# Kernel optimization log

Measured on AMD Instinct MI355X. Metric: run time of the kernel, lower is better.

## Reference

```python
import jax, jax.numpy as jnp
import numpy as np

NUM_HEADS = 12
LN_EPS = 1e-5


def _layernorm(x, w, b):
    m = jnp.mean(x, axis=-1, keepdims=True)
    v = jnp.mean(jnp.square(x - m), axis=-1, keepdims=True)
    return (x - m) * jax.lax.rsqrt(v + LN_EPS) * w + b


def setup_inputs() -> dict:
    key = jax.random.key(0)
    ks = jax.random.split(key, 6)
    B, N, C, H = 8, 1024, 768, 3072
    s = 0.02
    return {
        "x": jax.random.normal(ks[0], (B, N, C), jnp.float32),
        "ln1_w": jnp.ones((C,), jnp.float32),
        "ln1_b": jnp.zeros((C,), jnp.float32),
        "qkv_w": jax.random.normal(ks[1], (3 * C, C), jnp.float32) * s,
        "qkv_b": jnp.zeros((3 * C,), jnp.float32),
        "proj_w": jax.random.normal(ks[2], (C, C), jnp.float32) * s,
        "proj_b": jnp.zeros((C,), jnp.float32),
        "ln2_w": jnp.ones((C,), jnp.float32),
        "ln2_b": jnp.zeros((C,), jnp.float32),
        "fc1_w": jax.random.normal(ks[3], (H, C), jnp.float32) * s,
        "fc1_b": jnp.zeros((H,), jnp.float32),
        "fc2_w": jax.random.normal(ks[4], (C, H), jnp.float32) * s,
        "fc2_b": jnp.zeros((C,), jnp.float32),
    }


def reference(x, ln1_w, ln1_b, qkv_w, qkv_b, proj_w, proj_b,
              ln2_w, ln2_b, fc1_w, fc1_b, fc2_w, fc2_b):
    B, N, C = x.shape
    H = NUM_HEADS
    d = C // H
    scale = d ** (-0.5)

    # --- attention on norm1(x) (size=None path, dropout rates are 0) ---
    h = _layernorm(x, ln1_w, ln1_b)
    qkv = h @ qkv_w.T + qkv_b                      # [B,N,3C]
    qkv = qkv.reshape(B, N, 3, H, d).transpose(2, 0, 3, 1, 4)  # [3,B,H,N,d]
    q, k, v = qkv[0], qkv[1], qkv[2]
    attn = jnp.einsum('bhqd,bhkd->bhqk', q, k) * scale
    attn = jax.nn.softmax(attn, axis=-1)
    o = jnp.einsum('bhqk,bhkd->bhqd', attn, v)     # [B,H,N,d]
    o = o.transpose(0, 2, 1, 3).reshape(B, N, C)
    x_attn = o @ proj_w.T + proj_b

    # --- residual + MLP ---
    x = x + x_attn
    h2 = _layernorm(x, ln2_w, ln2_b)
    h2 = jax.nn.gelu(h2 @ fc1_w.T + fc1_b, approximate=False)
    x = x + (h2 @ fc2_w.T + fc2_b)
    return x
```

## Files before the change

### kernel.cpp

```cpp
#include <hip/hip_runtime.h>
#include <cmath>

typedef __bf16 bf16;
typedef __bf16 bf16x8 __attribute__((ext_vector_type(8)));
typedef __bf16 bf16x4 __attribute__((ext_vector_type(4)));
typedef float floatx4 __attribute__((ext_vector_type(4)));

#define MFMA16(A, B, C) __builtin_amdgcn_mfma_f32_16x16x32_bf16((A), (B), (C), 0, 0, 0)

#define GLDS16(g, l)                                                   \
  __builtin_amdgcn_global_load_lds(                                    \
      (const __attribute__((address_space(1))) void*)(g),              \
      (__attribute__((address_space(3))) void*)(l), 16, 0, 0)

__global__ __launch_bounds__(256) void pre_kernel(
    const float* __restrict__ x, const float* __restrict__ g,
    const float* __restrict__ be, bf16* __restrict__ h1,
    const float* __restrict__ s0, bf16* __restrict__ d0, int n0,
    const float* __restrict__ s1, bf16* __restrict__ d1, int n1,
    const float* __restrict__ s2, bf16* __restrict__ d2, int n2,
    const float* __restrict__ s3, bf16* __restrict__ d3, int n3) {
  int bid = blockIdx.x;
  int t = threadIdx.x;
  if (bid < 8192) {
    const float* xr = x + (size_t)bid * 768;
    float v0 = xr[t], v1 = xr[t + 256], v2 = xr[t + 512];
    float s = v0 + v1 + v2;
    float s2 = v0 * v0 + v1 * v1 + v2 * v2;
#pragma unroll
    for (int o = 1; o < 64; o <<= 1) {
      s += __shfl_xor(s, o, 64);
      s2 += __shfl_xor(s2, o, 64);
    }
    __shared__ float red[8];
    int w = t >> 6, lane = t & 63;
    if (lane == 0) { red[w] = s; red[4 + w] = s2; }
    __syncthreads();
    float ts = red[0] + red[1] + red[2] + red[3];
    float ts2 = red[4] + red[5] + red[6] + red[7];
    float mean = ts * (1.0f / 768.0f);
    float var = ts2 * (1.0f / 768.0f) - mean * mean;
    float rstd = rsqrtf(var + 1e-5f);
    bf16* orow = h1 + (size_t)bid * 768;
    orow[t]       = (bf16)((v0 - mean) * rstd * g[t]       + be[t]);
    orow[t + 256] = (bf16)((v1 - mean) * rstd * g[t + 256] + be[t + 256]);
    orow[t + 512] = (bf16)((v2 - mean) * rstd * g[t + 512] + be[t + 512]);
    return;
  }
  int i = (bid - 8192) * 256 + t;
  const float* s;
  bf16* d;
  if (i < n0) { s = s0 + (size_t)i * 4; d = d0 + (size_t)i * 4; }
  else if ((i -= n0) < n1) { s = s1 + (size_t)i * 4; d = d1 + (size_t)i * 4; }
  else if ((i -= n1) < n2) { s = s2 + (size_t)i * 4; d = d2 + (size_t)i * 4; }
  else if ((i -= n2) < n3) { s = s3 + (size_t)i * 4; d = d3 + (size_t)i * 4; }
  else return;
  bf16x4 v;
  v[0] = (bf16)s[0]; v[1] = (bf16)s[1]; v[2] = (bf16)s[2]; v[3] = (bf16)s[3];
  *(bf16x4*)d = v;
}

__global__ __launch_bounds__(256) void reduce_ln_kernel(
    const bf16* __restrict__ pp, const float* __restrict__ bias,
    const float* __restrict__ x, const float* __restrict__ g,
    const float* __restrict__ be, float* __restrict__ x1,
    bf16* __restrict__ h2) {
  int row = blockIdx.x;
  int t = threadIdx.x;
  const bf16* p0 = pp + (size_t)row * 768;
  const bf16* p1 = pp + (size_t)(8192 + row) * 768;
  const float* xr = x + (size_t)row * 768;
  float v0 = (float)p0[t]       + (float)p1[t]       + bias[t]       + xr[t];
  float v1 = (float)p0[t + 256] + (float)p1[t + 256] + bias[t + 256] + xr[t + 256];
  float v2 = (float)p0[t + 512] + (float)p1[t + 512] + bias[t + 512] + xr[t + 512];
  float* x1r = x1 + (size_t)row * 768;
  x1r[t] = v0; x1r[t + 256] = v1; x1r[t + 512] = v2;
  float s = v0 + v1 + v2;
  float s2 = v0 * v0 + v1 * v1 + v2 * v2;
#pragma unroll
  for (int o = 1; o < 64; o <<= 1) {
    s += __shfl_xor(s, o, 64);
    s2 += __shfl_xor(s2, o, 64);
  }
  __shared__ float red[8];
  int w = t >> 6, lane = t & 63;
  if (lane == 0) { red[w] = s; red[4 + w] = s2; }
  __syncthreads();
  float ts = red[0] + red[1] + red[2] + red[3];
  float ts2 = red[4] + red[5] + red[6] + red[7];
  float mean = ts * (1.0f / 768.0f);
  float var = ts2 * (1.0f / 768.0f) - mean * mean;
  float rstd = rsqrtf(var + 1e-5f);
  bf16* orow = h2 + (size_t)row * 768;
  orow[t]       = (bf16)((v0 - mean) * rstd * g[t]       + be[t]);
  orow[t + 256] = (bf16)((v1 - mean) * rstd * g[t + 256] + be[t + 256]);
  orow[t + 512] = (bf16)((v2 - mean) * rstd * g[t + 512] + be[t + 512]);
}

__global__ __launch_bounds__(256) void reduce_out_kernel(
    const bf16* __restrict__ pp, const float* __restrict__ bias,
    const float* __restrict__ x1, float* __restrict__ out) {
  int i = blockIdx.x * 256 + threadIdx.x;
  size_t base = (size_t)i * 4;
  int col = (int)(base % 768);
  bf16x4 a = *(const bf16x4*)(pp + base);
  bf16x4 b = *(const bf16x4*)(pp + (size_t)8192 * 768 + base);
  float4 xr = *(const float4*)(x1 + base);
  float4 r;
  r.x = (float)a[0] + (float)b[0] + bias[col]     + xr.x;
  r.y = (float)a[1] + (float)b[1] + bias[col + 1] + xr.y;
  r.z = (float)a[2] + (float)b[2] + bias[col + 2] + xr.z;
  r.w = (float)a[3] + (float)b[3] + bias[col + 3] + xr.w;
  *(float4*)(out + base) = r;
}

constexpr int EP_BF16 = 0;
constexpr int EP_PART = 1;
constexpr int EP_GELU_BF16 = 2;

template <int EP>
__global__ __launch_bounds__(256, 3) void gemm_bt(
    const bf16* __restrict__ A, const bf16* __restrict__ Bw,
    const float* __restrict__ bias,
    void* __restrict__ outp, int M, int N, int K) {
  __shared__ alignas(16) bf16 Asl[128 * 64];
  __shared__ alignas(16) bf16 Bsl[128 * 64];
  int tid = threadIdx.x;
  int lane = tid & 63, w = tid >> 6;
  int wm = w >> 1, wn = w & 1;
  int q16 = lane & 15, quad = lane >> 4;
  int fid = blockIdx.x + gridDim.x * blockIdx.y;
  int nb = gridDim.x;
  int s = fid >> 3;
  int m0 = ((fid & 7) * (gridDim.y >> 3) + s / nb) * 128;
  int n0 = (s % nb) * 128;
  int kz = blockIdx.z;
  int Ksub = K / gridDim.z;
  int kbeg = kz * Ksub;

  floatx4 acc[4][4];
#pragma unroll
  for (int i = 0; i < 4; i++)
#pragma unroll
    for (int j = 0; j < 4; j++) acc[i][j] = (floatx4){0.f, 0.f, 0.f, 0.f};

  int rIn = lane >> 3;
  int cg = (lane & 7) ^ rIn;
  const bf16* ag[4];
  const bf16* bg[4];
#pragma unroll
  for (int q = 0; q < 4; q++) {
    int ca = w * 4 + q;
    ag[q] = A + (size_t)(m0 + ca * 8 + rIn) * K + kbeg + cg * 8;
    bg[q] = Bw + (size_t)(n0 + ca * 8 + rIn) * K + kbeg + cg * 8;
  }
  bf16* la = &Asl[w * 2048];
  bf16* lb = &Bsl[w * 2048];

  int msel = q16 & 7;
  int offA[2][4], offB[2][4];
#pragma unroll
  for (int ks = 0; ks < 2; ks++) {
#pragma unroll
    for (int i = 0; i < 4; i++) {
      offA[ks][i] = (wm * 64 + i * 16 + q16) * 64 + (((ks * 4 + quad) ^ msel)) * 8;
      offB[ks][i] = (wn * 64 + i * 16 + q16) * 64 + (((ks * 4 + quad) ^ msel)) * 8;
    }
  }

  for (int k0 = 0; k0 < Ksub; k0 += 64) {
    __syncthreads();
#pragma unroll
    for (int q = 0; q < 4; q++) {
      GLDS16(ag[q], la + q * 512);
      GLDS16(bg[q], lb + q * 512);
      ag[q] += 64;
      bg[q] += 64;
    }
    __syncthreads();
#pragma unroll
    for (int ks = 0; ks < 2; ks++) {
      bf16x8 af[4], bfr[4];
#pragma unroll
      for (int i = 0; i < 4; i++) af[i] = *(const bf16x8*)&Asl[offA[ks][i]];
#pragma unroll
      for (int j = 0; j < 4; j++) bfr[j] = *(const bf16x8*)&Bsl[offB[ks][j]];
#pragma unroll
      for (int i = 0; i < 4; i++)
#pragma unroll
        for (int j = 0; j < 4; j++) acc[i][j] = MFMA16(af[i], bfr[j], acc[i][j]);
    }
  }

  bf16* opart = (bf16*)outp + (size_t)kz * M * N;
#pragma unroll
  for (int i = 0; i < 4; i++) {
#pragma unroll
    for (int j = 0; j < 4; j++) {
#pragma unroll
      for (int r = 0; r < 4; r++) {
        int m = m0 + wm * 64 + i * 16 + quad * 4 + r;
        int n = n0 + wn * 64 + j * 16 + q16;
        size_t idx = (size_t)m * N + n;
        if constexpr (EP == EP_PART) {
          opart[idx] = (bf16)acc[i][j][r];
        } else {
          float v = acc[i][j][r] + bias[n];
          if constexpr (EP == EP_BF16) {
            ((bf16*)outp)[idx] = (bf16)v;
          } else {
            float u = v * (2.3022083f + 0.1029443f * v * v);
            float e = __builtin_amdgcn_exp2f(-u);
            float gv = v * __builtin_amdgcn_rcpf(1.0f + e);
            ((bf16*)outp)[idx] = (bf16)gv;
          }
        }
      }
    }
  }
}

__global__ __launch_bounds__(256, 3) void attn_kernel(const bf16* __restrict__ qkv,
                                                      bf16* __restrict__ o) {
  __shared__ alignas(16) bf16 Kl[32 * 64];
  __shared__ alignas(16) bf16 Vt[64 * 5 * 8];
  __shared__ alignas(16) bf16 Pl[4][2][16 * 40];
  int tid = threadIdx.x;
  int lane = tid & 63, w = tid >> 6;
  int q16 = lane & 15, quad = lane >> 4;
  int b = blockIdx.y / 12, h = blockIdx.y % 12;
  int qbase = blockIdx.x * 128 + w * 32;

  bf16x8 qf[2][2];
#pragma unroll
  for (int qt = 0; qt < 2; qt++)
#pragma unroll
    for (int c = 0; c < 2; c++)
      qf[qt][c] = *(const bf16x8*)(qkv +
          (size_t)(b * 1024 + qbase + qt * 16 + q16) * 2304 + h * 64 +
          c * 32 + quad * 8);

  int kkey = w * 8 + (lane >> 3);
  int kchunk = (lane & 7) ^ (lane >> 3);
  const bf16* kg = qkv + (size_t)(b * 1024 + kkey) * 2304 + 768 + h * 64 +
                   (kchunk & 7) * 8;
  bf16* kl_dst = &Kl[w * 512];

  int kr = tid >> 3;
  int kcb = (tid & 7) * 8;
  const bf16* vg = qkv + (size_t)(b * 1024 + kr) * 2304 + 1536 + h * 64 + kcb;
  int vt_idx[8];
#pragma unroll
  for (int e = 0; e < 8; e++)
    vt_idx[e] = ((((kcb + e) * 5) + w) ^ (tid & 7)) * 8 + (kr & 7);

  int koff[2][2];
#pragma unroll
  for (int nc = 0; nc < 2; nc++)
#pragma unroll
    for (int ck = 0; ck < 2; ck++) {
      int key = nc * 16 + q16;
      koff[nc][ck] = (key * 8 + ((ck * 4 + quad) ^ (key & 7))) * 8;
    }
  int voff[4];
#pragma unroll
  for (int dc = 0; dc < 4; dc++) {
    int d = dc * 16 + q16;
    voff[dc] = ((d * 5 + quad) ^ ((d >> 3) & 7)) * 8;
  }
  const bf16* pread = &Pl[w][0][q16 * 40 + quad * 8];
  int pw_base = (quad * 4) * 40 + q16;

  float l_[2][4];
  floatx4 oacc[2][4];
#pragma unroll
  for (int qt = 0; qt < 2; qt++)
#pragma unroll
    for (int r = 0; r < 4; r++) l_[qt][r] = 0.f;
#pragma unroll
  for (int qt = 0; qt < 2; qt++)
#pragma unroll
    for (int dc = 0; dc < 4; dc++) oacc[qt][dc] = (floatx4){0.f, 0.f, 0.f, 0.f};

  for (int kt = 0; kt < 32; kt++) {
    __syncthreads();
    GLDS16(kg, kl_dst);
    bf16x8 vv = *(const bf16x8*)vg;
    kg += 32 * 2304;
    vg += 32 * 2304;
#pragma unroll
    for (int e = 0; e < 8; e++) Vt[vt_idx[e]] = vv[e];
    __syncthreads();

    bf16x8 kf[2][2];
#pragma unroll
    for (int nc = 0; nc < 2; nc++)
#pragma unroll
      for (int ck = 0; ck < 2; ck++)
        kf[nc][ck] = *(const bf16x8*)&Kl[koff[nc][ck]];

#pragma unroll
    for (int qt = 0; qt < 2; qt++) {
#pragma unroll
      for (int nc = 0; nc < 2; nc++) {
        floatx4 z = (floatx4){0.f, 0.f, 0.f, 0.f};
        z = MFMA16(qf[qt][0], kf[nc][0], z);
        z = MFMA16(qf[qt][1], kf[nc][1], z);
#pragma unroll
        for (int r = 0; r < 4; r++) {
          float p = __builtin_amdgcn_exp2f(z[r] * 0.18033688011f);
          l_[qt][r] += p;
          Pl[w][qt][pw_base + r * 40 + nc * 16] = (bf16)p;
        }
      }
    }
    __syncthreads();

    bf16x8 vf[4];
#pragma unroll
    for (int dc = 0; dc < 4; dc++) vf[dc] = *(const bf16x8*)&Vt[voff[dc]];
#pragma unroll
    for (int qt = 0; qt < 2; qt++) {
      bf16x8 pf = *(const bf16x8*)(pread + qt * 640);
#pragma unroll
      for (int dc = 0; dc < 4; dc++)
        oacc[qt][dc] = MFMA16(pf, vf[dc], oacc[qt][dc]);
    }
  }

#pragma unroll
  for (int qt = 0; qt < 2; qt++) {
    bf16* op = o + (size_t)(b * 1024 + qbase + qt * 16) * 768 + h * 64;
#pragma unroll
    for (int r = 0; r < 4; r++) {
      float s = l_[qt][r];
#pragma unroll
      for (int off = 1; off < 16; off <<= 1) s += __shfl_xor(s, off, 16);
      float inv = 1.0f / s;
#pragma unroll
      for (int dc = 0; dc < 4; dc++)
        op[(size_t)(quad * 4 + r) * 768 + dc * 16 + q16] =
            (bf16)(oacc[qt][dc][r] * inv);
    }
  }
}

extern "C" void kernel_launch(void* const* d_in, const int* in_sizes, int n_in,
                              void* d_out, int out_size, void* d_ws, size_t ws_size,
                              hipStream_t stream) {
  (void)in_sizes; (void)n_in; (void)out_size; (void)ws_size;
  const float* x      = (const float*)d_in[0];
  const float* ln1_w  = (const float*)d_in[1];
  const float* ln1_b  = (const float*)d_in[2];
  const float* qkv_w  = (const float*)d_in[3];
  const float* qkv_b  = (const float*)d_in[4];
  const float* proj_w = (const float*)d_in[5];
  const float* proj_b = (const float*)d_in[6];
  const float* ln2_w  = (const float*)d_in[7];
  const float* ln2_b  = (const float*)d_in[8];
  const float* fc1_w  = (const float*)d_in[9];
  const float* fc1_b  = (const float*)d_in[10];
  const float* fc2_w  = (const float*)d_in[11];
  const float* fc2_b  = (const float*)d_in[12];

  char* ws = (char*)d_ws;
  size_t off = 0;
  auto alloc = [&](size_t bytes) {
    void* p = ws + off;
    off += (bytes + 255) & ~(size_t)255;
    return p;
  };
  bf16* wq  = (bf16*)alloc((size_t)2304 * 768 * 2);
  bf16* wp  = (bf16*)alloc((size_t)768 * 768 * 2);
  bf16* wf1 = (bf16*)alloc((size_t)3072 * 768 * 2);
  bf16* wf2 = (bf16*)alloc((size_t)768 * 3072 * 2);
  bf16* slotA = (bf16*)alloc((size_t)8192 * 768 * 2);
  bf16* slotB = (bf16*)alloc((size_t)8192 * 3072 * 2);
  float* x1 = (float*)alloc((size_t)8192 * 768 * 4);
  bf16* part = (bf16*)alloc((size_t)2 * 8192 * 768 * 2);

  bf16* h1 = slotA;
  bf16* qkvb = slotB;
  bf16* ob = slotA;
  bf16* h2 = slotA;
  bf16* hm = slotB;

  pre_kernel<<<8192 + 6912, 256, 0, stream>>>(
      x, ln1_w, ln1_b, h1,
      qkv_w, wq, 2304 * 768 / 4, proj_w, wp, 768 * 768 / 4,
      fc1_w, wf1, 3072 * 768 / 4, fc2_w, wf2, 768 * 3072 / 4);

  gemm_bt<EP_BF16><<<dim3(18, 64, 1), 256, 0, stream>>>(h1, wq, qkv_b, qkvb,
                                                        8192, 2304, 768);
  attn_kernel<<<dim3(8, 96), 256, 0, stream>>>(qkvb, ob);
  gemm_bt<EP_PART><<<dim3(6, 64, 2), 256, 0, stream>>>(ob, wp, nullptr, part,
                                                       8192, 768, 768);
  reduce_ln_kernel<<<8192, 256, 0, stream>>>(part, proj_b, x, ln2_w, ln2_b,
                                             x1, h2);
  gemm_bt<EP_GELU_BF16><<<dim3(24, 64, 1), 256, 0, stream>>>(h2, wf1, fc1_b, hm,
                                                             8192, 3072, 768);
  gemm_bt<EP_PART><<<dim3(6, 64, 2), 256, 0, stream>>>(hm, wf2, nullptr, part,
                                                       8192, 768, 3072);
  reduce_out_kernel<<<6144, 256, 0, stream>>>(part, fc2_b, x1, (float*)d_out);
}
```

Baseline: 334.2 us.

## Replace split-K partials with 128x64 tiles, fuse residual epilogue, widen attention KV tile

The proj and fc2 GEMMs drop split-K, which wrote bf16 partials that a separate reduce kernel then summed. They now use 128x64 output tiles, templated via NJ, so the grid stays large, and add bias plus residual in the epilogue, writing fp32 directly. The reduce kernels are removed, leaving a plain LayerNorm kernel on x1. Attention now processes 64 keys per iteration with double K/V buffers, removes one barrier per step, and remaps blocks so each batch sits on one XCD. Risks are lower arithmetic intensity from the narrower tiles, and possible races on the P buffer now that the barrier between P write and read is gone, though each warp reads only its own region.

Measured after the change: 332.2 us. About the same (-0.6%).

```diff
diff --git a/kernel.cpp b/kernel.cpp
--- a/kernel.cpp
+++ b/kernel.cpp
@@ -60,21 +60,14 @@
   *(bf16x4*)d = v;
 }
 
-__global__ __launch_bounds__(256) void reduce_ln_kernel(
-    const bf16* __restrict__ pp, const float* __restrict__ bias,
-    const float* __restrict__ x, const float* __restrict__ g,
-    const float* __restrict__ be, float* __restrict__ x1,
-    bf16* __restrict__ h2) {
+__global__ __launch_bounds__(256) void ln_kernel(const float* __restrict__ x,
+                                                 const float* __restrict__ g,
+                                                 const float* __restrict__ be,
+                                                 bf16* __restrict__ out) {
   int row = blockIdx.x;
   int t = threadIdx.x;
-  const bf16* p0 = pp + (size_t)row * 768;
-  const bf16* p1 = pp + (size_t)(8192 + row) * 768;
   const float* xr = x + (size_t)row * 768;
-  float v0 = (float)p0[t]       + (float)p1[t]       + bias[t]       + xr[t];
-  float v1 = (float)p0[t + 256] + (float)p1[t + 256] + bias[t + 256] + xr[t + 256];
-  float v2 = (float)p0[t + 512] + (float)p1[t + 512] + bias[t + 512] + xr[t + 512];
-  float* x1r = x1 + (size_t)row * 768;
-  x1r[t] = v0; x1r[t + 256] = v1; x1r[t + 512] = v2;
+  float v0 = xr[t], v1 = xr[t + 256], v2 = xr[t + 512];
   float s = v0 + v1 + v2;
   float s2 = v0 * v0 + v1 * v1 + v2 * v2;
 #pragma unroll
@@ -91,40 +84,23 @@
   float mean = ts * (1.0f / 768.0f);
   float var = ts2 * (1.0f / 768.0f) - mean * mean;
   float rstd = rsqrtf(var + 1e-5f);
-  bf16* orow = h2 + (size_t)row * 768;
+  bf16* orow = out + (size_t)row * 768;
   orow[t]       = (bf16)((v0 - mean) * rstd * g[t]       + be[t]);
   orow[t + 256] = (bf16)((v1 - mean) * rstd * g[t + 256] + be[t + 256]);
   orow[t + 512] = (bf16)((v2 - mean) * rstd * g[t + 512] + be[t + 512]);
 }
 
-__global__ __launch_bounds__(256) void reduce_out_kernel(
-    const bf16* __restrict__ pp, const float* __restrict__ bias,
-    const float* __restrict__ x1, float* __restrict__ out) {
-  int i = blockIdx.x * 256 + threadIdx.x;
-  size_t base = (size_t)i * 4;
-  int col = (int)(base % 768);
-  bf16x4 a = *(const bf16x4*)(pp + base);
-  bf16x4 b = *(const bf16x4*)(pp + (size_t)8192 * 768 + base);
-  float4 xr = *(const float4*)(x1 + base);
-  float4 r;
-  r.x = (float)a[0] + (float)b[0] + bias[col]     + xr.x;
-  r.y = (float)a[1] + (float)b[1] + bias[col + 1] + xr.y;
-  r.z = (float)a[2] + (float)b[2] + bias[col + 2] + xr.z;
-  r.w = (float)a[3] + (float)b[3] + bias[col + 3] + xr.w;
-  *(float4*)(out + base) = r;
-}
-
 constexpr int EP_BF16 = 0;
-constexpr int EP_PART = 1;
+constexpr int EP_RES_F32 = 1;
 constexpr int EP_GELU_BF16 = 2;
 
-template <int EP>
+template <int EP, int NJ>
 __global__ __launch_bounds__(256, 3) void gemm_bt(
     const bf16* __restrict__ A, const bf16* __restrict__ Bw,
-    const float* __restrict__ bias,
+    const float* __restrict__ bias, const float* __restrict__ resid,
     void* __restrict__ outp, int M, int N, int K) {
   __shared__ alignas(16) bf16 Asl[128 * 64];
-  __shared__ alignas(16) bf16 Bsl[128 * 64];
+  __shared__ alignas(16) bf16 Bsl[NJ * 32 * 64];
   int tid = threadIdx.x;
   int lane = tid & 63, w = tid >> 6;
   int wm = w >> 1, wn = w & 1;
@@ -133,87 +109,85 @@
   int nb = gridDim.x;
   int s = fid >> 3;
   int m0 = ((fid & 7) * (gridDim.y >> 3) + s / nb) * 128;
-  int n0 = (s % nb) * 128;
-  int kz = blockIdx.z;
-  int Ksub = K / gridDim.z;
-  int kbeg = kz * Ksub;
-
-  floatx4 acc[4][4];
+  int n0 = (s % nb) * (NJ * 32);
+
+  floatx4 acc[4][NJ];
 #pragma unroll
   for (int i = 0; i < 4; i++)
 #pragma unroll
-    for (int j = 0; j < 4; j++) acc[i][j] = (floatx4){0.f, 0.f, 0.f, 0.f};
+    for (int j = 0; j < NJ; j++) acc[i][j] = (floatx4){0.f, 0.f, 0.f, 0.f};
 
   int rIn = lane >> 3;
   int cg = (lane & 7) ^ rIn;
   const bf16* ag[4];
-  const bf16* bg[4];
-#pragma unroll
-  for (int q = 0; q < 4; q++) {
-    int ca = w * 4 + q;
-    ag[q] = A + (size_t)(m0 + ca * 8 + rIn) * K + kbeg + cg * 8;
-    bg[q] = Bw + (size_t)(n0 + ca * 8 + rIn) * K + kbeg + cg * 8;
-  }
+  const bf16* bg[NJ];
+#pragma unroll
+  for (int q = 0; q < 4; q++)
+    ag[q] = A + (size_t)(m0 + (w * 4 + q) * 8 + rIn) * K + cg * 8;
+#pragma unroll
+  for (int q = 0; q < NJ; q++)
+    bg[q] = Bw + (size_t)(n0 + (w * NJ + q) * 8 + rIn) * K + cg * 8;
   bf16* la = &Asl[w * 2048];
-  bf16* lb = &Bsl[w * 2048];
+  bf16* lb = &Bsl[w * NJ * 512];
 
   int msel = q16 & 7;
-  int offA[2][4], offB[2][4];
+  int offA[2][4], offB[2][NJ];
 #pragma unroll
   for (int ks = 0; ks < 2; ks++) {
 #pragma unroll
-    for (int i = 0; i < 4; i++) {
+    for (int i = 0; i < 4; i++)
       offA[ks][i] = (wm * 64 + i * 16 + q16) * 64 + (((ks * 4 + quad) ^ msel)) * 8;
-      offB[ks][i] = (wn * 64 + i * 16 + q16) * 64 + (((ks * 4 + quad) ^ msel)) * 8;
-    }
-  }
-
-  for (int k0 = 0; k0 < Ksub; k0 += 64) {
+#pragma unroll
+    for (int j = 0; j < NJ; j++)
+      offB[ks][j] = (wn * 16 * NJ + j * 16 + q16) * 64 + (((ks * 4 + quad) ^ msel)) * 8;
+  }
+
+  for (int k0 = 0; k0 < K; k0 += 64) {
     __syncthreads();
 #pragma unroll
     for (int q = 0; q < 4; q++) {
       GLDS16(ag[q], la + q * 512);
+      ag[q] += 64;
+    }
+#pragma unroll
+    for (int q = 0; q < NJ; q++) {
       GLDS16(bg[q], lb + q * 512);
-      ag[q] += 64;
       bg[q] += 64;
     }
     __syncthreads();
 #pragma unroll
     for (int ks = 0; ks < 2; ks++) {
-      bf16x8 af[4], bfr[4];
+      bf16x8 af[4], bfr[NJ];
 #pragma unroll
       for (int i = 0; i < 4; i++) af[i] = *(const bf16x8*)&Asl[offA[ks][i]];
 #pragma unroll
-      for (int j = 0; j < 4; j++) bfr[j] = *(const bf16x8*)&Bsl[offB[ks][j]];
+      for (int j = 0; j < NJ; j++) bfr[j] = *(const bf16x8*)&Bsl[offB[ks][j]];
 #pragma unroll
       for (int i = 0; i < 4; i++)
 #pragma unroll
-        for (int j = 0; j < 4; j++) acc[i][j] = MFMA16(af[i], bfr[j], acc[i][j]);
-    }
-  }
-
-  bf16* opart = (bf16*)outp + (size_t)kz * M * N;
+        for (int j = 0; j < NJ; j++) acc[i][j] = MFMA16(af[i], bfr[j], acc[i][j]);
+    }
+  }
+
 #pragma unroll
   for (int i = 0; i < 4; i++) {
 #pragma unroll
-    for (int j = 0; j < 4; j++) {
+    for (int j = 0; j < NJ; j++) {
 #pragma unroll
       for (int r = 0; r < 4; r++) {
         int m = m0 + wm * 64 + i * 16 + quad * 4 + r;
-        int n = n0 + wn * 64 + j * 16 + q16;
+        int n = n0 + wn * 16 * NJ + j * 16 + q16;
         size_t idx = (size_t)m * N + n;
-        if constexpr (EP == EP_PART) {
-          opart[idx] = (bf16)acc[i][j][r];
+        float v = acc[i][j][r] + bias[n];
+        if constexpr (EP == EP_BF16) {
+          ((bf16*)outp)[idx] = (bf16)v;
+        } else if constexpr (EP == EP_RES_F32) {
+          ((float*)outp)[idx] = v + resid[idx];
         } else {
-          float v = acc[i][j][r] + bias[n];
-          if constexpr (EP == EP_BF16) {
-            ((bf16*)outp)[idx] = (bf16)v;
-          } else {
-            float u = v * (2.3022083f + 0.1029443f * v * v);
-            float e = __builtin_amdgcn_exp2f(-u);
-            float gv = v * __builtin_amdgcn_rcpf(1.0f + e);
-            ((bf16*)outp)[idx] = (bf16)gv;
-          }
+          float u = v * (2.3022083f + 0.1029443f * v * v);
+          float e = __builtin_amdgcn_exp2f(-u);
+          float gv = v * __builtin_amdgcn_rcpf(1.0f + e);
+          ((bf16*)outp)[idx] = (bf16)gv;
         }
       }
     }
@@ -222,14 +196,16 @@
 
 __global__ __launch_bounds__(256, 3) void attn_kernel(const bf16* __restrict__ qkv,
                                                       bf16* __restrict__ o) {
-  __shared__ alignas(16) bf16 Kl[32 * 64];
-  __shared__ alignas(16) bf16 Vt[64 * 5 * 8];
-  __shared__ alignas(16) bf16 Pl[4][2][16 * 40];
+  __shared__ alignas(16) bf16 Kl[2][32 * 64];
+  __shared__ alignas(16) bf16 Vt[2][64 * 40];
+  __shared__ alignas(16) bf16 Pl[4][2][16 * 68];
   int tid = threadIdx.x;
   int lane = tid & 63, w = tid >> 6;
   int q16 = lane & 15, quad = lane >> 4;
-  int b = blockIdx.y / 12, h = blockIdx.y % 12;
-  int qbase = blockIdx.x * 128 + w * 32;
+  int f = blockIdx.x;
+  int xcd = f & 7, idx = f >> 3;
+  int b = xcd, h = idx % 12;
+  int qbase = (idx / 12) * 128 + w * 32;
 
   bf16x8 qf[2][2];
 #pragma unroll
@@ -242,17 +218,20 @@
 
   int kkey = w * 8 + (lane >> 3);
   int kchunk = (lane & 7) ^ (lane >> 3);
-  const bf16* kg = qkv + (size_t)(b * 1024 + kkey) * 2304 + 768 + h * 64 +
-                   (kchunk & 7) * 8;
-  bf16* kl_dst = &Kl[w * 512];
+  const bf16* kg0 = qkv + (size_t)(b * 1024 + kkey) * 2304 + 768 + h * 64 +
+                    kchunk * 8;
+  const bf16* kg1 = kg0 + 32 * 2304;
+  bf16* kd0 = &Kl[0][w * 512];
+  bf16* kd1 = &Kl[1][w * 512];
 
   int kr = tid >> 3;
   int kcb = (tid & 7) * 8;
-  const bf16* vg = qkv + (size_t)(b * 1024 + kr) * 2304 + 1536 + h * 64 + kcb;
+  const bf16* vg0 = qkv + (size_t)(b * 1024 + kr) * 2304 + 1536 + h * 64 + kcb;
+  const bf16* vg1 = vg0 + 32 * 2304;
   int vt_idx[8];
 #pragma unroll
   for (int e = 0; e < 8; e++)
-    vt_idx[e] = ((((kcb + e) * 5) + w) ^ (tid & 7)) * 8 + (kr & 7);
+    vt_idx[e] = ((((kcb + e) * 5) + (kr >> 3)) ^ (tid & 7)) * 8 + (kr & 7);
 
   int koff[2][2];
 #pragma unroll
@@ -268,8 +247,8 @@
     int d = dc * 16 + q16;
     voff[dc] = ((d * 5 + quad) ^ ((d >> 3) & 7)) * 8;
   }
-  const bf16* pread = &Pl[w][0][q16 * 40 + quad * 8];
-  int pw_base = (quad * 4) * 40 + q16;
+  const bf16* pread = &Pl[w][0][q16 * 68 + quad * 8];
+  int pw_base = (quad * 4) * 68 + q16;
 
   float l_[2][4];
   floatx4 oacc[2][4];
@@ -282,27 +261,31 @@
 #pragma unroll
     for (int dc = 0; dc < 4; dc++) oacc[qt][dc] = (floatx4){0.f, 0.f, 0.f, 0.f};
 
-  for (int kt = 0; kt < 32; kt++) {
-    __syncthreads();
-    GLDS16(kg, kl_dst);
-    bf16x8 vv = *(const bf16x8*)vg;
-    kg += 32 * 2304;
-    vg += 32 * 2304;
-#pragma unroll
-    for (int e = 0; e < 8; e++) Vt[vt_idx[e]] = vv[e];
-    __syncthreads();
-
-    bf16x8 kf[2][2];
-#pragma unroll
-    for (int nc = 0; nc < 2; nc++)
+  for (int kt = 0; kt < 16; kt++) {
+    __syncthreads();
+    GLDS16(kg0, kd0);
+    GLDS16(kg1, kd1);
+    bf16x8 vv0 = *(const bf16x8*)vg0;
+    bf16x8 vv1 = *(const bf16x8*)vg1;
+    kg0 += 64 * 2304; kg1 += 64 * 2304;
+    vg0 += 64 * 2304; vg1 += 64 * 2304;
+#pragma unroll
+    for (int e = 0; e < 8; e++) Vt[0][vt_idx[e]] = vv0[e];
+#pragma unroll
+    for (int e = 0; e < 8; e++) Vt[1][vt_idx[e]] = vv1[e];
+    __syncthreads();
+
+    bf16x8 kf[4][2];
+#pragma unroll
+    for (int nc = 0; nc < 4; nc++)
 #pragma unroll
       for (int ck = 0; ck < 2; ck++)
-        kf[nc][ck] = *(const bf16x8*)&Kl[koff[nc][ck]];
+        kf[nc][ck] = *(const bf16x8*)&Kl[nc >> 1][koff[nc & 1][ck]];
 
 #pragma unroll
     for (int qt = 0; qt < 2; qt++) {
 #pragma unroll
-      for (int nc = 0; nc < 2; nc++) {
+      for (int nc = 0; nc < 4; nc++) {
         floatx4 z = (floatx4){0.f, 0.f, 0.f, 0.f};
         z = MFMA16(qf[qt][0], kf[nc][0], z);
         z = MFMA16(qf[qt][1], kf[nc][1], z);
@@ -310,21 +293,26 @@
         for (int r = 0; r < 4; r++) {
           float p = __builtin_amdgcn_exp2f(z[r] * 0.18033688011f);
           l_[qt][r] += p;
-          Pl[w][qt][pw_base + r * 40 + nc * 16] = (bf16)p;
+          Pl[w][qt][pw_base + r * 68 + nc * 16] = (bf16)p;
         }
       }
     }
-    __syncthreads();
-
-    bf16x8 vf[4];
-#pragma unroll
-    for (int dc = 0; dc < 4; dc++) vf[dc] = *(const bf16x8*)&Vt[voff[dc]];
+
+    bf16x8 vf[2][4];
+#pragma unroll
+    for (int kh = 0; kh < 2; kh++)
+#pragma unroll
+      for (int dc = 0; dc < 4; dc++)
+        vf[kh][dc] = *(const bf16x8*)&Vt[kh][voff[dc]];
 #pragma unroll
     for (int qt = 0; qt < 2; qt++) {
-      bf16x8 pf = *(const bf16x8*)(pread + qt * 640);
-#pragma unroll
-      for (int dc = 0; dc < 4; dc++)
-        oacc[qt][dc] = MFMA16(pf, vf[dc], oacc[qt][dc]);
+#pragma unroll
+      for (int kh = 0; kh < 2; kh++) {
+        bf16x8 pf = *(const bf16x8*)(pread + qt * 1088 + kh * 32);
+#pragma unroll
+        for (int dc = 0; dc < 4; dc++)
+          oacc[qt][dc] = MFMA16(pf, vf[kh][dc], oacc[qt][dc]);
+      }
     }
   }
 
@@ -377,7 +365,6 @@
   bf16* slotA = (bf16*)alloc((size_t)8192 * 768 * 2);
   bf16* slotB = (bf16*)alloc((size_t)8192 * 3072 * 2);
   float* x1 = (float*)alloc((size_t)8192 * 768 * 4);
-  bf16* part = (bf16*)alloc((size_t)2 * 8192 * 768 * 2);
 
   bf16* h1 = slotA;
   bf16* qkvb = slotB;
@@ -390,16 +377,14 @@
       qkv_w, wq, 2304 * 768 / 4, proj_w, wp, 768 * 768 / 4,
       fc1_w, wf1, 3072 * 768 / 4, fc2_w, wf2, 768 * 3072 / 4);
 
-  gemm_bt<EP_BF16><<<dim3(18, 64, 1), 256, 0, stream>>>(h1, wq, qkv_b, qkvb,
-                                                        8192, 2304, 768);
-  attn_kernel<<<dim3(8, 96), 256, 0, stream>>>(qkvb, ob);
-  gemm_bt<EP_PART><<<dim3(6, 64, 2), 256, 0, stream>>>(ob, wp, nullptr, part,
-                                                       8192, 768, 768);
-  reduce_ln_kernel<<<8192, 256, 0, stream>>>(part, proj_b, x, ln2_w, ln2_b,
-                                             x1, h2);
-  gemm_bt<EP_GELU_BF16><<<dim3(24, 64, 1), 256, 0, stream>>>(h2, wf1, fc1_b, hm,
-                                                             8192, 3072, 768);
-  gemm_bt<EP_PART><<<dim3(6, 64, 2), 256, 0, stream>>>(hm, wf2, nullptr, part,
-                                                       8192, 768, 3072);
-  reduce_out_kernel<<<6144, 256, 0, stream>>>(part, fc2_b, x1, (float*)d_out);
-}
+  gemm_bt<EP_BF16, 4><<<dim3(18, 64), 256, 0, stream>>>(
+      h1, wq, qkv_b, nullptr, qkvb, 8192, 2304, 768);
+  attn_kernel<<<768, 256, 0, stream>>>(qkvb, ob);
+  gemm_bt<EP_RES_F32, 2><<<dim3(12, 64), 256, 0, stream>>>(
+      ob, wp, proj_b, x, x1, 8192, 768, 768);
+  ln_kernel<<<8192, 256, 0, stream>>>(x1, ln2_w, ln2_b, h2);
+  gemm_bt<EP_GELU_BF16, 4><<<dim3(24, 64), 256, 0, stream>>>(
+      h2, wf1, fc1_b, nullptr, hm, 8192, 3072, 768);
+  gemm_bt<EP_RES_F32, 2><<<dim3(12, 64), 256, 0, stream>>>(
+      hm, wf2, fc2_b, x1, (float*)d_out, 8192, 768, 3072);
+}
```
